# Optimization experiments

Measured on AMD Instinct MI355X. Metric: run time of the kernel, lower is better.

The kernel has to match this reference:

```python
import jax, jax.numpy as jnp
import numpy as np

EMBEDDING_DIM = 64
N_EMBEDDINGS = 512


def setup_inputs() -> dict:
    key = jax.random.key(0)
    k1, k2 = jax.random.split(key)
    inputs = jax.random.normal(k1, (32, 64, 64, 64), dtype=jnp.float32)  # NCHW, C==embedding_dim
    weight = jax.random.normal(k2, (N_EMBEDDINGS, EMBEDDING_DIM), dtype=jnp.float32)
    return {"inputs": inputs, "weight": weight}


def reference(inputs, weight):
    # NCHW -> NHWC, flatten to [N, D]
    x = jnp.transpose(inputs, (0, 2, 3, 1))  # [B, H, W, D]
    in_shape = x.shape
    flat = x.reshape(-1, EMBEDDING_DIM)  # [N, D]

    distances = (
        jnp.sum(flat * flat, axis=1, keepdims=True)
        + jnp.sum(weight * weight, axis=1)
        - 2.0 * flat @ weight.T
    )
    idx = jnp.argmin(distances, axis=1)  # [N]

    # one-hot @ weight is just a gather
    quantized = weight[idx].reshape(in_shape)  # [B, H, W, D]

    # commitment loss: mse(stop_grad(quantized), x)
    e_latent_loss = jnp.mean(jnp.square(jax.lax.stop_gradient(quantized) - x))

    # straight-through estimator
    quantized = x + jax.lax.stop_gradient(quantized - x)

    return jnp.transpose(quantized, (0, 3, 1, 2)), e_latent_loss
```

## Files before the change

### kernel.cpp

```cpp
#include <hip/hip_runtime.h>
#include <math.h>

typedef short bf16x8 __attribute__((ext_vector_type(8)));
typedef float f32x4 __attribute__((ext_vector_type(4)));

#define VQ_D 64
#define VQ_K 512
#define VQ_NQ 131072
#define VQ_TOTAL 8388608
#define NCK 8
#define TAU 8e-3f

typedef __attribute__((address_space(1))) void as1_void;
typedef __attribute__((address_space(3))) void as3_void;

__device__ __forceinline__ void gll16(const void* g, void* l) {
    __builtin_amdgcn_global_load_lds((as1_void*)(void*)g, (as3_void*)l, 16, 0, 0);
}
__device__ __forceinline__ void gll4(const void* g, void* l) {
    __builtin_amdgcn_global_load_lds((as1_void*)(void*)g, (as3_void*)l, 4, 0, 0);
}

__device__ __forceinline__ ushort bf16_rne(float f) {
    uint u = __builtin_bit_cast(uint, f);
    u += 0x7fffu + ((u >> 16) & 1u);
    return (ushort)(u >> 16);
}
__device__ __forceinline__ float bf16_to_f(ushort h) {
    uint u = ((uint)h) << 16;
    return __builtin_bit_cast(float, u);
}
__device__ __forceinline__ uint rne_top(float r) {
    uint t = __builtin_bit_cast(uint, r);
    return t + 0x7fffu + ((t >> 16) & 1u);
}
__device__ __forceinline__ uint pack_hi16(uint a, uint b) {
    return __builtin_amdgcn_perm(b, a, 0x07060302u);
}

__global__ __launch_bounds__(128) void vq_prep(const float* __restrict__ w,
                                               ushort* __restrict__ wfrag,
                                               float* __restrict__ wn,
                                               float* __restrict__ out) {
    if (blockIdx.x == 0 && threadIdx.x == 0) out[VQ_TOTAL] = 0.f;
    const int tid = threadIdx.x;
    const int k = (blockIdx.x << 4) + (tid >> 3);
    const int g = tid & 7;
    const float4* row = (const float4*)(w + k * VQ_D);
    float4 a = row[2 * g], b4 = row[2 * g + 1];
    float v[8] = {a.x, a.y, a.z, a.w, b4.x, b4.y, b4.z, b4.w};
    ushort hi[8], lo[8];
    float nrm = 0.f;
#pragma unroll
    for (int j = 0; j < 8; ++j) {
        nrm = fmaf(v[j], v[j], nrm);
        hi[j] = bf16_rne(v[j]);
        lo[j] = bf16_rne(v[j] - bf16_to_f(hi[j]));
    }
    nrm += __shfl_xor(nrm, 1, 64);
    nrm += __shfl_xor(nrm, 2, 64);
    nrm += __shfl_xor(nrm, 4, 64);
    if (g == 0) wn[k] = nrm;
    const int t = k >> 4, col = k & 15;
    const int quad = g & 3, fh = g >> 2;
    bf16x8* basez = (bf16x8*)wfrag + t * 256 + quad * 16 + col;
    basez[fh * 64]       = *(bf16x8*)hi;
    basez[(2 + fh) * 64] = *(bf16x8*)lo;
}

__global__ __launch_bounds__(512, 8) void vq_main(const float* __restrict__ in,
                                                  const float* __restrict__ w,
                                                  const ushort* __restrict__ wfrag,
                                                  const float* __restrict__ wng,
                                                  float* __restrict__ out) {
    __shared__ __align__(16) char bstage[2][16384];
    __shared__ float wn_lds[VQ_K];
    __shared__ float xn_lds[128];
    __shared__ float best_lds[128], sec_lds[128];
    __shared__ int   bi_lds[128], si_lds[128];
    __shared__ double loss_lds[8];

    const int tid  = threadIdx.x;
    const int lane = tid & 63;
    const int wid  = tid >> 6;
    const int col  = lane & 15;
    const int quad = lane >> 4;
    const int n0  = blockIdx.x * 128;
    const int b   = n0 >> 12;
    const int hw0 = n0 & 4095;
    const float* xg0 = in + (b << 18) + hw0;

    {
        const char* gs = (const char*)wfrag + tid * 16;
        char* lb = &bstage[0][0] + wid * 1024;
        gll16(gs, lb);
        gll16(gs + 8192, lb + 8192);
        gll4(wng + tid, (char*)wn_lds + wid * 256);
    }

    bf16x8 ah0, ah1, al0, al1;
    {
        const float* xq = xg0 + wid * 16 + col;
        float sx = 0.f;
        uint AH0[4], AL0[4], AH1[4], AL1[4];
#pragma unroll
        for (int m = 0; m < 4; ++m) {
            float a0 = xq[(quad * 8 + 2 * m) << 12];
            float b0 = xq[(quad * 8 + 2 * m + 1) << 12];
            float a1 = xq[(32 + quad * 8 + 2 * m) << 12];
            float b1 = xq[(32 + quad * 8 + 2 * m + 1) << 12];
            sx = fmaf(a0, a0, sx); sx = fmaf(b0, b0, sx);
            sx = fmaf(a1, a1, sx); sx = fmaf(b1, b1, sx);
            uint ua0 = __builtin_bit_cast(uint, a0), ub0 = __builtin_bit_cast(uint, b0);
            uint ua1 = __builtin_bit_cast(uint, a1), ub1 = __builtin_bit_cast(uint, b1);
            AH0[m] = pack_hi16(ua0, ub0);
            AH1[m] = pack_hi16(ua1, ub1);
            float ha0 = __builtin_bit_cast(float, ua0 & 0xFFFF0000u);
            float hb0 = __builtin_bit_cast(float, ub0 & 0xFFFF0000u);
            float ha1 = __builtin_bit_cast(float, ua1 & 0xFFFF0000u);
            float hb1 = __builtin_bit_cast(float, ub1 & 0xFFFF0000u);
            AL0[m] = pack_hi16(rne_top(a0 - ha0), rne_top(b0 - hb0));
            AL1[m] = pack_hi16(rne_top(a1 - ha1), rne_top(b1 - hb1));
        }
        ah0 = *(bf16x8*)AH0; al0 = *(bf16x8*)AL0;
        ah1 = *(bf16x8*)AH1; al1 = *(bf16x8*)AL1;
        sx += __shfl_xor(sx, 16, 64);
        sx += __shfl_xor(sx, 32, 64);
        if (quad == 0) xn_lds[wid * 16 + col] = sx;
    }

    __syncthreads();

    float best[4], sec[4];
#pragma unroll
    for (int r = 0; r < 4; ++r) { best[r] = 3.0e38f; sec[r] = 3.0e38f; }

#pragma unroll 1
    for (int c = 0; c < NCK; ++c) {
        char* const bcur = &bstage[c & 1][0];
        if (c + 1 < NCK) {
            const char* gs = (const char*)wfrag + (c + 1) * 16384 + tid * 16;
            char* lb = &bstage[(c + 1) & 1][0] + wid * 1024;
            gll16(gs, lb);
            gll16(gs + 8192, lb + 8192);
        }
#pragma unroll
        for (int s = 0; s < 4; ++s) {
            const int t2 = 4 * c + s;
            const char* rb = bcur + s * 4096 + lane * 16;
            bf16x8 bh0 = *(const bf16x8*)(rb);
            bf16x8 bh1 = *(const bf16x8*)(rb + 1024);
            bf16x8 bl0 = *(const bf16x8*)(rb + 2048);
            bf16x8 bl1 = *(const bf16x8*)(rb + 3072);
            const float wnv = wn_lds[t2 * 16 + col];
            f32x4 acc = {0.f, 0.f, 0.f, 0.f};
            acc = __builtin_amdgcn_mfma_f32_16x16x32_bf16(ah0, bh0, acc, 0, 0, 0);
            acc = __builtin_amdgcn_mfma_f32_16x16x32_bf16(ah1, bh1, acc, 0, 0, 0);
            acc = __builtin_amdgcn_mfma_f32_16x16x32_bf16(ah0, bl0, acc, 0, 0, 0);
            acc = __builtin_amdgcn_mfma_f32_16x16x32_bf16(ah1, bl1, acc, 0, 0, 0);
            acc = __builtin_amdgcn_mfma_f32_16x16x32_bf16(al0, bh0, acc, 0, 0, 0);
            acc = __builtin_amdgcn_mfma_f32_16x16x32_bf16(al1, bh1, acc, 0, 0, 0);
#pragma unroll
            for (int j = 0; j < 4; ++j) {
                float dist = fmaf(-2.f, acc[j], wnv);
                uint u = (__builtin_bit_cast(uint, dist) & 0xFFFFFFE0u)
                       | ((uint)t2 & 0x1Fu);
                float key = __builtin_bit_cast(float, u);
                sec[j]  = __builtin_amdgcn_fmed3f(best[j], sec[j], key);
                best[j] = fminf(best[j], key);
            }
        }
        __syncthreads();
    }

    float bD[4], sD[4];
    int bI[4], sI[4];
#pragma unroll
    for (int r = 0; r < 4; ++r) {
        uint ub = __builtin_bit_cast(uint, best[r]);
        uint us = __builtin_bit_cast(uint, sec[r]);
        bI[r] = (int)(ub & 31u) * 16 + col;
        sI[r] = (int)(us & 31u) * 16 + col;
        bD[r] = __builtin_bit_cast(float, ub & 0xFFFFFFE0u);
        sD[r] = __builtin_bit_cast(float, us & 0xFFFFFFE0u);
    }

#pragma unroll
    for (int off = 1; off < 16; off <<= 1) {
#pragma unroll
        for (int r = 0; r < 4; ++r) {
            float ob = __shfl_xor(bD[r], off, 64);
            float os = __shfl_xor(sD[r], off, 64);
            int   oi = __shfl_xor(bI[r], off, 64);
            int   oc = __shfl_xor(sI[r], off, 64);
            bool oWins = (ob < bD[r]) || (ob == bD[r] && oi < bI[r]);
            float nb  = oWins ? ob    : bD[r];
            int   ni  = oWins ? oi    : bI[r];
            float c1  = oWins ? bD[r] : ob;
            int   ci1 = oWins ? bI[r] : oi;
            float c2  = oWins ? os    : sD[r];
            int   ci2 = oWins ? oc    : sI[r];
            bool c1w = (c1 < c2) || (c1 == c2 && ci1 < ci2);
            sD[r] = c1w ? c1  : c2;
            sI[r] = c1w ? ci1 : ci2;
            bD[r] = nb; bI[r] = ni;
        }
    }
    if (col == 0) {
#pragma unroll
        for (int r = 0; r < 4; ++r) {
            const int q = wid * 16 + quad * 4 + r;
            best_lds[q] = bD[r]; sec_lds[q] = sD[r];
            bi_lds[q] = bI[r];   si_lds[q] = sI[r];
        }
    }
    __syncthreads();

    {
        const int q = tid >> 2, part = tid & 3;
        float cb = best_lds[q], cs = sec_lds[q];
        int cbi = bi_lds[q], csi = si_lds[q];
        double chosen = (double)cb;
        if (cs - cb < TAU) {
            const float* wb  = w + cbi * VQ_D + part * 16;
            const float* ws2 = w + csi * VQ_D + part * 16;
            const float* xqp = xg0 + q;
            double nb = 0.0, dotb = 0.0, ns = 0.0, dots = 0.0;
#pragma unroll
            for (int d0 = 0; d0 < 16; ++d0) {
                const int d = part * 16 + d0;
                double xv = (double)xqp[d << 12];
                double wbv = (double)wb[d0], wsv = (double)ws2[d0];
                nb = fma(wbv, wbv, nb); dotb = fma(xv, wbv, dotb);
                ns = fma(wsv, wsv, ns); dots = fma(xv, wsv, dots);
            }
#pragma unroll
            for (int off = 1; off < 4; off <<= 1) {
                nb   += __shfl_xor(nb,   off, 64);
                dotb += __shfl_xor(dotb, off, 64);
                ns   += __shfl_xor(ns,   off, 64);
                dots += __shfl_xor(dots, off, 64);
            }
            double db = nb - 2.0 * dotb, ds = ns - 2.0 * dots;
            if (ds < db || (ds == db && csi < cbi)) { cbi = csi; chosen = ds; }
            else                                    { chosen = db; }
        }
        if (part == 0) bi_lds[q] = cbi;
        double lq = (part == 0) ? ((double)xn_lds[q] + chosen) : 0.0;
#pragma unroll
        for (int off = 32; off > 0; off >>= 1)
            lq += __shfl_down(lq, off, 64);
        if (lane == 0) loss_lds[wid] = lq;
    }
    __syncthreads();
    if (tid == 0) {
        double s = 0.0;
#pragma unroll
        for (int wv = 0; wv < 8; ++wv) s += loss_lds[wv];
        atomicAdd(out + VQ_TOTAL, (float)(s * (1.0 / (double)VQ_TOTAL)));
    }

    {
        const int q = tid & 127, quarter = tid >> 7;
        const float4* wrow = (const float4*)(w + bi_lds[q] * VQ_D) + quarter * 4;
        float* op = out + (b << 18) + hw0 + q;
#pragma unroll
        for (int u = 0; u < 4; ++u) {
            float4 v = wrow[u];
            const int d = quarter * 16 + 4 * u;
            op[(d + 0) << 12] = v.x;
            op[(d + 1) << 12] = v.y;
            op[(d + 2) << 12] = v.z;
            op[(d + 3) << 12] = v.w;
        }
    }
}

extern "C" void kernel_launch(void* const* d_in, const int* in_sizes, int n_in,
                              void* d_out, int out_size, void* d_ws, size_t ws_size,
                              hipStream_t stream) {
    const float* in = (const float*)d_in[0];
    const float* w  = (const float*)d_in[1];
    float* out = (float*)d_out;

    ushort* wfrag = (ushort*)d_ws;
    float*  wn    = (float*)((char*)d_ws + 131072);

    vq_prep<<<32, 128, 0, stream>>>(w, wfrag, wn, out);
    vq_main<<<VQ_NQ / 128, 512, 0, stream>>>(in, w, wfrag, wn, out);
}
```

Measured before the change: 115.6 us.

## Fuse codebook bf16 split prep into main VQ kernel with register prefetch

Removes the separate prep kernel that converted the codebook into hi/lo bf16 MFMA fragments and norms in workspace. Each block of the main kernel now loads raw fp32 codebook rows into registers, converts them and writes the fragments and norms straight into LDS, double-buffered so the conversion of one chunk overlaps the MFMA work on the other. This saves a kernel launch and the workspace round trip, but every one of the 1024 blocks now repeats the conversion arithmetic. The loss accumulator is cleared with a memset instead of inside the prep kernel.

```diff
diff --git a/kernel.cpp b/kernel.cpp
--- a/kernel.cpp
+++ b/kernel.cpp
@@ -8,18 +8,7 @@
 #define VQ_K 512
 #define VQ_NQ 131072
 #define VQ_TOTAL 8388608
-#define NCK 8
 #define TAU 8e-3f
-
-typedef __attribute__((address_space(1))) void as1_void;
-typedef __attribute__((address_space(3))) void as3_void;
-
-__device__ __forceinline__ void gll16(const void* g, void* l) {
-    __builtin_amdgcn_global_load_lds((as1_void*)(void*)g, (as3_void*)l, 16, 0, 0);
-}
-__device__ __forceinline__ void gll4(const void* g, void* l) {
-    __builtin_amdgcn_global_load_lds((as1_void*)(void*)g, (as3_void*)l, 4, 0, 0);
-}
 
 __device__ __forceinline__ ushort bf16_rne(float f) {
     uint u = __builtin_bit_cast(uint, f);
@@ -38,16 +27,10 @@
     return __builtin_amdgcn_perm(b, a, 0x07060302u);
 }
 
-__global__ __launch_bounds__(128) void vq_prep(const float* __restrict__ w,
-                                               ushort* __restrict__ wfrag,
-                                               float* __restrict__ wn,
-                                               float* __restrict__ out) {
-    if (blockIdx.x == 0 && threadIdx.x == 0) out[VQ_TOTAL] = 0.f;
-    const int tid = threadIdx.x;
-    const int k = (blockIdx.x << 4) + (tid >> 3);
-    const int g = tid & 7;
-    const float4* row = (const float4*)(w + k * VQ_D);
-    float4 a = row[2 * g], b4 = row[2 * g + 1];
+__device__ __forceinline__ void conv_chunk(float4 a, float4 b4, int tid, int chunk,
+                                           char* buf, float* wn_lds) {
+    const int ci = tid >> 3;
+    const int g  = tid & 7;
     float v[8] = {a.x, a.y, a.z, a.w, b4.x, b4.y, b4.z, b4.w};
     ushort hi[8], lo[8];
     float nrm = 0.f;
@@ -60,19 +43,17 @@
     nrm += __shfl_xor(nrm, 1, 64);
     nrm += __shfl_xor(nrm, 2, 64);
     nrm += __shfl_xor(nrm, 4, 64);
-    if (g == 0) wn[k] = nrm;
-    const int t = k >> 4, col = k & 15;
+    if (g == 0) wn_lds[chunk * 64 + ci] = nrm;
+    const int s = ci >> 4, col = ci & 15;
     const int quad = g & 3, fh = g >> 2;
-    bf16x8* basez = (bf16x8*)wfrag + t * 256 + quad * 16 + col;
-    basez[fh * 64]       = *(bf16x8*)hi;
-    basez[(2 + fh) * 64] = *(bf16x8*)lo;
-}
-
-__global__ __launch_bounds__(512, 8) void vq_main(const float* __restrict__ in,
-                                                  const float* __restrict__ w,
-                                                  const ushort* __restrict__ wfrag,
-                                                  const float* __restrict__ wng,
-                                                  float* __restrict__ out) {
+    char* base = buf + s * 4096 + (quad * 16 + col) * 16;
+    *(bf16x8*)(base + fh * 1024)        = *(bf16x8*)hi;
+    *(bf16x8*)(base + 2048 + fh * 1024) = *(bf16x8*)lo;
+}
+
+__global__ __launch_bounds__(512, 8) void vq_fused(const float* __restrict__ in,
+                                                   const float* __restrict__ w,
+                                                   float* __restrict__ out) {
     __shared__ __align__(16) char bstage[2][16384];
     __shared__ float wn_lds[VQ_K];
     __shared__ float xn_lds[128];
@@ -90,13 +71,11 @@
     const int hw0 = n0 & 4095;
     const float* xg0 = in + (b << 18) + hw0;
 
-    {
-        const char* gs = (const char*)wfrag + tid * 16;
-        char* lb = &bstage[0][0] + wid * 1024;
-        gll16(gs, lb);
-        gll16(gs + 8192, lb + 8192);
-        gll4(wng + tid, (char*)wn_lds + wid * 256);
-    }
+    const int wci = tid >> 3, wg = tid & 7;
+    const float4* p0 = (const float4*)(w + (0 * 64 + wci) * VQ_D) + 2 * wg;
+    float4 wa0 = p0[0], wa1 = p0[1];
+    const float4* p1 = (const float4*)(w + (1 * 64 + wci) * VQ_D) + 2 * wg;
+    float4 wb0 = p1[0], wb1 = p1[1];
 
     bf16x8 ah0, ah1, al0, al1;
     {
@@ -129,49 +108,61 @@
         if (quad == 0) xn_lds[wid * 16 + col] = sx;
     }
 
+    conv_chunk(wa0, wa1, tid, 0, &bstage[0][0], wn_lds);
     __syncthreads();
 
     float best[4], sec[4];
 #pragma unroll
     for (int r = 0; r < 4; ++r) { best[r] = 3.0e38f; sec[r] = 3.0e38f; }
 
+#define VQ_COMPUTE(T2BASE, BUF)                                                   \
+    {                                                                             \
+        _Pragma("unroll")                                                         \
+        for (int s = 0; s < 4; ++s) {                                             \
+            const int t2 = (T2BASE) + s;                                          \
+            const char* rb = (BUF) + s * 4096 + lane * 16;                        \
+            bf16x8 bh0 = *(const bf16x8*)(rb);                                    \
+            bf16x8 bh1 = *(const bf16x8*)(rb + 1024);                             \
+            bf16x8 bl0 = *(const bf16x8*)(rb + 2048);                             \
+            bf16x8 bl1 = *(const bf16x8*)(rb + 3072);                             \
+            const float wnv = wn_lds[t2 * 16 + col];                              \
+            f32x4 acc = {0.f, 0.f, 0.f, 0.f};                                     \
+            acc = __builtin_amdgcn_mfma_f32_16x16x32_bf16(ah0, bh0, acc, 0, 0, 0);\
+            acc = __builtin_amdgcn_mfma_f32_16x16x32_bf16(ah1, bh1, acc, 0, 0, 0);\
+            acc = __builtin_amdgcn_mfma_f32_16x16x32_bf16(ah0, bl0, acc, 0, 0, 0);\
+            acc = __builtin_amdgcn_mfma_f32_16x16x32_bf16(ah1, bl1, acc, 0, 0, 0);\
+            acc = __builtin_amdgcn_mfma_f32_16x16x32_bf16(al0, bh0, acc, 0, 0, 0);\
+            acc = __builtin_amdgcn_mfma_f32_16x16x32_bf16(al1, bh1, acc, 0, 0, 0);\
+            _Pragma("unroll")                                                     \
+            for (int j = 0; j < 4; ++j) {                                         \
+                float dist = fmaf(-2.f, acc[j], wnv);                             \
+                uint u = (__builtin_bit_cast(uint, dist) & 0xFFFFFFE0u)           \
+                       | ((uint)t2 & 0x1Fu);                                      \
+                float key = __builtin_bit_cast(float, u);                         \
+                sec[j]  = __builtin_amdgcn_fmed3f(best[j], sec[j], key);          \
+                best[j] = fminf(best[j], key);                                    \
+            }                                                                     \
+        }                                                                         \
+    }
+
 #pragma unroll 1
-    for (int c = 0; c < NCK; ++c) {
-        char* const bcur = &bstage[c & 1][0];
-        if (c + 1 < NCK) {
-            const char* gs = (const char*)wfrag + (c + 1) * 16384 + tid * 16;
-            char* lb = &bstage[(c + 1) & 1][0] + wid * 1024;
-            gll16(gs, lb);
-            gll16(gs + 8192, lb + 8192);
-        }
-#pragma unroll
-        for (int s = 0; s < 4; ++s) {
-            const int t2 = 4 * c + s;
-            const char* rb = bcur + s * 4096 + lane * 16;
-            bf16x8 bh0 = *(const bf16x8*)(rb);
-            bf16x8 bh1 = *(const bf16x8*)(rb + 1024);
-            bf16x8 bl0 = *(const bf16x8*)(rb + 2048);
-            bf16x8 bl1 = *(const bf16x8*)(rb + 3072);
-            const float wnv = wn_lds[t2 * 16 + col];
-            f32x4 acc = {0.f, 0.f, 0.f, 0.f};
-            acc = __builtin_amdgcn_mfma_f32_16x16x32_bf16(ah0, bh0, acc, 0, 0, 0);
-            acc = __builtin_amdgcn_mfma_f32_16x16x32_bf16(ah1, bh1, acc, 0, 0, 0);
-            acc = __builtin_amdgcn_mfma_f32_16x16x32_bf16(ah0, bl0, acc, 0, 0, 0);
-            acc = __builtin_amdgcn_mfma_f32_16x16x32_bf16(ah1, bl1, acc, 0, 0, 0);
-            acc = __builtin_amdgcn_mfma_f32_16x16x32_bf16(al0, bh0, acc, 0, 0, 0);
-            acc = __builtin_amdgcn_mfma_f32_16x16x32_bf16(al1, bh1, acc, 0, 0, 0);
-#pragma unroll
-            for (int j = 0; j < 4; ++j) {
-                float dist = fmaf(-2.f, acc[j], wnv);
-                uint u = (__builtin_bit_cast(uint, dist) & 0xFFFFFFE0u)
-                       | ((uint)t2 & 0x1Fu);
-                float key = __builtin_bit_cast(float, u);
-                sec[j]  = __builtin_amdgcn_fmed3f(best[j], sec[j], key);
-                best[j] = fminf(best[j], key);
-            }
-        }
+    for (int i = 0; i < 4; ++i) {
+        conv_chunk(wb0, wb1, tid, 2 * i + 1, &bstage[1][0], wn_lds);
+        if (i < 3) {
+            const float4* p = (const float4*)(w + ((2 * i + 2) * 64 + wci) * VQ_D) + 2 * wg;
+            wa0 = p[0]; wa1 = p[1];
+        }
+        VQ_COMPUTE(4 * (2 * i), &bstage[0][0]);
         __syncthreads();
-    }
+        if (i < 3) {
+            conv_chunk(wa0, wa1, tid, 2 * i + 2, &bstage[0][0], wn_lds);
+            const float4* p = (const float4*)(w + ((2 * i + 3) * 64 + wci) * VQ_D) + 2 * wg;
+            wb0 = p[0]; wb1 = p[1];
+        }
+        VQ_COMPUTE(4 * (2 * i + 1), &bstage[1][0]);
+        __syncthreads();
+    }
+#undef VQ_COMPUTE
 
     float bD[4], sD[4];
     int bI[4], sI[4];
@@ -283,9 +274,6 @@
     const float* w  = (const float*)d_in[1];
     float* out = (float*)d_out;
 
-    ushort* wfrag = (ushort*)d_ws;
-    float*  wn    = (float*)((char*)d_ws + 131072);
-
-    vq_prep<<<32, 128, 0, stream>>>(w, wfrag, wn, out);
-    vq_main<<<VQ_NQ / 128, 512, 0, stream>>>(in, w, wfrag, wn, out);
-}
+    hipMemsetAsync(out + VQ_TOTAL, 0, 4, stream);
+    vq_fused<<<VQ_NQ / 128, 512, 0, stream>>>(in, w, out);
+}
```

Result: slower. 187.7 us (+62.4%).

## Fuse codebook bf16 split conversion into main kernel, drop prep launch

Applied to the files above, without the earlier changes.

The separate prep kernel, which split the codebook into bf16 hi/lo fragments and computed norms, is removed. Each block of the main kernel now loads raw fp32 codebook chunks, converts them in registers and writes them into the double-buffered LDS stage, prefetching the next chunk while the current one is computed. This removes a kernel launch and the workspace round trip. In exchange, all 1024 blocks repeat the conversion work, the async global-to-LDS loads become register loads, and the loss accumulator is zeroed with a memset.

```diff
diff --git a/kernel.cpp b/kernel.cpp
--- a/kernel.cpp
+++ b/kernel.cpp
@@ -8,18 +8,7 @@
 #define VQ_K 512
 #define VQ_NQ 131072
 #define VQ_TOTAL 8388608
-#define NCK 8
 #define TAU 8e-3f
-
-typedef __attribute__((address_space(1))) void as1_void;
-typedef __attribute__((address_space(3))) void as3_void;
-
-__device__ __forceinline__ void gll16(const void* g, void* l) {
-    __builtin_amdgcn_global_load_lds((as1_void*)(void*)g, (as3_void*)l, 16, 0, 0);
-}
-__device__ __forceinline__ void gll4(const void* g, void* l) {
-    __builtin_amdgcn_global_load_lds((as1_void*)(void*)g, (as3_void*)l, 4, 0, 0);
-}
 
 __device__ __forceinline__ ushort bf16_rne(float f) {
     uint u = __builtin_bit_cast(uint, f);
@@ -38,43 +27,11 @@
     return __builtin_amdgcn_perm(b, a, 0x07060302u);
 }
 
-__global__ __launch_bounds__(128) void vq_prep(const float* __restrict__ w,
-                                               ushort* __restrict__ wfrag,
-                                               float* __restrict__ wn,
-                                               float* __restrict__ out) {
-    if (blockIdx.x == 0 && threadIdx.x == 0) out[VQ_TOTAL] = 0.f;
-    const int tid = threadIdx.x;
-    const int k = (blockIdx.x << 4) + (tid >> 3);
-    const int g = tid & 7;
-    const float4* row = (const float4*)(w + k * VQ_D);
-    float4 a = row[2 * g], b4 = row[2 * g + 1];
-    float v[8] = {a.x, a.y, a.z, a.w, b4.x, b4.y, b4.z, b4.w};
-    ushort hi[8], lo[8];
-    float nrm = 0.f;
-#pragma unroll
-    for (int j = 0; j < 8; ++j) {
-        nrm = fmaf(v[j], v[j], nrm);
-        hi[j] = bf16_rne(v[j]);
-        lo[j] = bf16_rne(v[j] - bf16_to_f(hi[j]));
-    }
-    nrm += __shfl_xor(nrm, 1, 64);
-    nrm += __shfl_xor(nrm, 2, 64);
-    nrm += __shfl_xor(nrm, 4, 64);
-    if (g == 0) wn[k] = nrm;
-    const int t = k >> 4, col = k & 15;
-    const int quad = g & 3, fh = g >> 2;
-    bf16x8* basez = (bf16x8*)wfrag + t * 256 + quad * 16 + col;
-    basez[fh * 64]       = *(bf16x8*)hi;
-    basez[(2 + fh) * 64] = *(bf16x8*)lo;
-}
-
-__global__ __launch_bounds__(512, 8) void vq_main(const float* __restrict__ in,
-                                                  const float* __restrict__ w,
-                                                  const ushort* __restrict__ wfrag,
-                                                  const float* __restrict__ wng,
-                                                  float* __restrict__ out) {
+__global__ __launch_bounds__(512, 8) void vq_fused(const float* __restrict__ in,
+                                                   const float* __restrict__ w,
+                                                   float* __restrict__ out) {
     __shared__ __align__(16) char bstage[2][16384];
-    __shared__ float wn_lds[VQ_K];
+    __shared__ float wn_a[VQ_K], wn_b[VQ_K];
     __shared__ float xn_lds[128];
     __shared__ float best_lds[128], sec_lds[128];
     __shared__ int   bi_lds[128], si_lds[128];
@@ -90,12 +47,37 @@
     const int hw0 = n0 & 4095;
     const float* xg0 = in + (b << 18) + hw0;
 
-    {
-        const char* gs = (const char*)wfrag + tid * 16;
-        char* lb = &bstage[0][0] + wid * 1024;
-        gll16(gs, lb);
-        gll16(gs + 8192, lb + 8192);
-        gll4(wng + tid, (char*)wn_lds + wid * 256);
+    const int cs  = tid >> 7;
+    const int cfh = (tid >> 6) & 1;
+    const int cgOff = (cs * 16 + col) * 64 + (cfh * 4 + quad) * 8;
+    float* wn_half = cfh ? wn_b : wn_a;
+
+    char* const cwbase0 = &bstage[0][0] + cs * 4096 + cfh * 1024 + lane * 16;
+    char* const cwbase1 = &bstage[1][0] + cs * 4096 + cfh * 1024 + lane * 16;
+
+#define VQ_CONV(A4, B4, CHUNK, CWBASE)                                            \
+    {                                                                             \
+        float v[8] = {(A4).x, (A4).y, (A4).z, (A4).w,                             \
+                      (B4).x, (B4).y, (B4).z, (B4).w};                            \
+        ushort hi[8], lo[8];                                                      \
+        float nrm = 0.f;                                                          \
+        _Pragma("unroll")                                                         \
+        for (int j = 0; j < 8; ++j) {                                             \
+            nrm = fmaf(v[j], v[j], nrm);                                          \
+            hi[j] = bf16_rne(v[j]);                                               \
+            lo[j] = bf16_rne(v[j] - bf16_to_f(hi[j]));                            \
+        }                                                                         \
+        nrm += __shfl_xor(nrm, 16, 64);              \
+        nrm += __shfl_xor(nrm, 32, 64);           \
+        if (quad == 0) wn_half[(CHUNK) * 64 + cs * 16 + col] = nrm;               \
+        *(bf16x8*)(CWBASE)        = *(bf16x8*)hi;                    \
+        *(bf16x8*)((CWBASE) + 2048) = *(bf16x8*)lo;                  \
+    }
+
+    float4 wr0, wr1;
+    {
+        const float4* p = (const float4*)(w + cgOff);
+        wr0 = p[0]; wr1 = p[1];
     }
 
     bf16x8 ah0, ah1, al0, al1;
@@ -129,6 +111,7 @@
         if (quad == 0) xn_lds[wid * 16 + col] = sx;
     }
 
+    VQ_CONV(wr0, wr1, 0, cwbase0);
     __syncthreads();
 
     float best[4], sec[4];
@@ -136,14 +119,13 @@
     for (int r = 0; r < 4; ++r) { best[r] = 3.0e38f; sec[r] = 3.0e38f; }
 
 #pragma unroll 1
-    for (int c = 0; c < NCK; ++c) {
-        char* const bcur = &bstage[c & 1][0];
-        if (c + 1 < NCK) {
-            const char* gs = (const char*)wfrag + (c + 1) * 16384 + tid * 16;
-            char* lb = &bstage[(c + 1) & 1][0] + wid * 1024;
-            gll16(gs, lb);
-            gll16(gs + 8192, lb + 8192);
-        }
+    for (int c = 0; c < 8; ++c) {
+        float4 nx0, nx1;
+        if (c < 7) {
+            const float4* p = (const float4*)(w + (c + 1) * 4096 + cgOff);
+            nx0 = p[0]; nx1 = p[1];
+        }
+        const char* bcur = &bstage[c & 1][0];
 #pragma unroll
         for (int s = 0; s < 4; ++s) {
             const int t2 = 4 * c + s;
@@ -152,7 +134,7 @@
             bf16x8 bh1 = *(const bf16x8*)(rb + 1024);
             bf16x8 bl0 = *(const bf16x8*)(rb + 2048);
             bf16x8 bl1 = *(const bf16x8*)(rb + 3072);
-            const float wnv = wn_lds[t2 * 16 + col];
+            const float wnv = wn_a[t2 * 16 + col] + wn_b[t2 * 16 + col];
             f32x4 acc = {0.f, 0.f, 0.f, 0.f};
             acc = __builtin_amdgcn_mfma_f32_16x16x32_bf16(ah0, bh0, acc, 0, 0, 0);
             acc = __builtin_amdgcn_mfma_f32_16x16x32_bf16(ah1, bh1, acc, 0, 0, 0);
@@ -170,8 +152,12 @@
                 best[j] = fminf(best[j], key);
             }
         }
+        if (c < 7) {
+            VQ_CONV(nx0, nx1, c + 1, ((c + 1) & 1) ? cwbase1 : cwbase0);
+        }
         __syncthreads();
     }
+#undef VQ_CONV
 
     float bD[4], sD[4];
     int bI[4], sI[4];
@@ -218,10 +204,10 @@
 
     {
         const int q = tid >> 2, part = tid & 3;
-        float cb = best_lds[q], cs = sec_lds[q];
+        float cb = best_lds[q], cs2 = sec_lds[q];
         int cbi = bi_lds[q], csi = si_lds[q];
         double chosen = (double)cb;
-        if (cs - cb < TAU) {
+        if (cs2 - cb < TAU) {
             const float* wb  = w + cbi * VQ_D + part * 16;
             const float* ws2 = w + csi * VQ_D + part * 16;
             const float* xqp = xg0 + q;
@@ -283,9 +269,6 @@
     const float* w  = (const float*)d_in[1];
     float* out = (float*)d_out;
 
-    ushort* wfrag = (ushort*)d_ws;
-    float*  wn    = (float*)((char*)d_ws + 131072);
-
-    vq_prep<<<32, 128, 0, stream>>>(w, wfrag, wn, out);
-    vq_main<<<VQ_NQ / 128, 512, 0, stream>>>(in, w, wfrag, wn, out);
-}
+    hipMemsetAsync(out + VQ_TOTAL, 0, 4, stream);
+    vq_fused<<<VQ_NQ / 128, 512, 0, stream>>>(in, w, out);
+}
```

New measurement: 175.1 us. 1.51x slower.
